# Performance work log

Hardware: AMD Instinct MI355X
Metric: run time of the kernel (lower is better)

Reference implementation:

```python
import jax, jax.numpy as jnp
import numpy as np

D_MODEL = 2048
N_HEADS = 16
HEAD_DIM = D_MODEL // N_HEADS  # 128


def setup_inputs() -> dict:
    key = jax.random.key(0)
    ks = jax.random.split(key, 7)
    B, S, CACHE = 2, 2048, 2048
    scale = 1.0 / np.sqrt(D_MODEL)
    return {
        "x": jax.random.normal(ks[0], (B, S, D_MODEL), dtype=jnp.float32),
        "cached_k": jax.random.normal(ks[1], (B, N_HEADS, CACHE, HEAD_DIM), dtype=jnp.float32),
        "cached_v": jax.random.normal(ks[2], (B, N_HEADS, CACHE, HEAD_DIM), dtype=jnp.float32),
        "W_q": jax.random.normal(ks[3], (D_MODEL, D_MODEL), dtype=jnp.float32) * scale,
        "W_k": jax.random.normal(ks[4], (D_MODEL, D_MODEL), dtype=jnp.float32) * scale,
        "W_v": jax.random.normal(ks[5], (D_MODEL, D_MODEL), dtype=jnp.float32) * scale,
        "W_o": jax.random.normal(ks[6], (D_MODEL, D_MODEL), dtype=jnp.float32) * scale,
    }


def reference(x, cached_k, cached_v, W_q, W_k, W_v, W_o):
    B, S, _ = x.shape
    # nn.Linear(d,d,bias=False): y = x @ W.T
    def proj(W):
        h = jnp.einsum("bsd,ed->bse", x, W)
        return h.reshape(B, S, N_HEADS, HEAD_DIM).transpose(0, 2, 1, 3)  # (B,H,S,Dh)
    q = proj(W_q)
    k = jnp.concatenate([cached_k, proj(W_k)], axis=2)  # (B,H,T,Dh)
    v = jnp.concatenate([cached_v, proj(W_v)], axis=2)
    scores = jnp.einsum("bhsd,bhtd->bhst", q, k) / np.sqrt(HEAD_DIM)
    attn = jax.nn.softmax(scores, axis=-1)
    out = jnp.einsum("bhst,bhtd->bhsd", attn, v)  # (B,H,S,Dh)
    out = out.transpose(0, 2, 1, 3).reshape(B, S, D_MODEL)
    out = jnp.einsum("bsd,ed->bse", out, W_o)
    return out, k, v
```

## Files before the change

### kernel.cpp

```cpp
#include <hip/hip_runtime.h>

typedef __bf16 bf16;
typedef __bf16 bf16x4 __attribute__((ext_vector_type(4)));
typedef __bf16 bf16x8 __attribute__((ext_vector_type(8)));
typedef float f32x4 __attribute__((ext_vector_type(4)));
typedef float f32x16 __attribute__((ext_vector_type(16)));
typedef int iv2 __attribute__((ext_vector_type(2)));

#define LOG2E 1.44269504088896340736f
#define QSCALE 0.12751884935f
#define RESCALE_THR 8.0f

__device__ __forceinline__ void gload_lds16(const void* gp, void* lp) {
    __builtin_amdgcn_global_load_lds(
        (__attribute__((address_space(1))) void*)gp,
        (__attribute__((address_space(3))) void*)lp,
        16, 0, 0);
}

__device__ __forceinline__ int kmask(int r) {
    return (r & 15) ^ (((r >> 5) & 1) << 2);
}

__device__ __forceinline__ unsigned cvtpk(float lo, float hi) {
    unsigned w;
    asm("v_cvt_pk_bf16_f32 %0, %1, %2" : "=v"(w) : "v"(lo), "v"(hi));
    return w;
}

__device__ __forceinline__ iv2 permswap(unsigned a, unsigned b) {
    return __builtin_amdgcn_permlane32_swap((int)a, (int)b, false, false);
}
__device__ __forceinline__ float halfmax(float v) {
    iv2 r = permswap(__float_as_uint(v), __float_as_uint(v));
    return fmaxf(__int_as_float(r[0]), __int_as_float(r[1]));
}
__device__ __forceinline__ float halfadd(float v) {
    iv2 r = permswap(__float_as_uint(v), __float_as_uint(v));
    return __int_as_float(r[0]) + __int_as_float(r[1]);
}

__device__ __forceinline__ float vmax32(const f32x16& a, const f32x16& b) {
    float t[8];
    #pragma unroll
    for (int i = 0; i < 8; ++i)
        t[i] = fmaxf(fmaxf(a[i], a[i + 8]), fmaxf(b[i], b[i + 8]));
    return fmaxf(fmaxf(fmaxf(t[0], t[1]), fmaxf(t[2], t[3])),
                 fmaxf(fmaxf(t[4], t[5]), fmaxf(t[6], t[7])));
}
__device__ __forceinline__ float vsum32(const f32x16& a, const f32x16& b) {
    float t[8];
    #pragma unroll
    for (int i = 0; i < 8; ++i)
        t[i] = (a[i] + a[i + 8]) + (b[i] + b[i + 8]);
    return ((t[0] + t[1]) + (t[2] + t[3])) + ((t[4] + t[5]) + (t[6] + t[7]));
}

__global__ void conv_all(const float* __restrict__ x, const float* __restrict__ wq,
                         const float* __restrict__ wk, const float* __restrict__ wv,
                         const float* __restrict__ wo, bf16* __restrict__ xb,
                         bf16* __restrict__ wbase) {
    int id = blockIdx.x;
    const float* src;
    bf16* dst;
    int i;
    if (id < 8192) {
        src = x; dst = xb;
        i = id * 256 + threadIdx.x;
    } else {
        int w = (id - 8192) >> 12;
        src = (w == 0) ? wq : (w == 1) ? wk : (w == 2) ? wv : wo;
        dst = wbase + (size_t)w * 4194304;
        i = ((id - 8192) & 4095) * 256 + threadIdx.x;
    }
    float4 f = ((const float4*)src)[i];
    bf16x4 v;
    v[0] = (bf16)f.x; v[1] = (bf16)f.y; v[2] = (bf16)f.z; v[3] = (bf16)f.w;
    *(bf16x4*)(dst + (size_t)i * 4) = v;
}

__global__ void copy_cache_k(const float* __restrict__ ck, float* __restrict__ kout,
                             bf16* __restrict__ kb) {
    size_t i = ((size_t)blockIdx.x * 256 + threadIdx.x) * 4;
    size_t bh  = i >> 18;
    size_t rem = i & 262143;
    size_t o   = (bh << 19) + rem;
    float4 f = *(const float4*)(ck + i);
    *(float4*)(kout + o) = f;
    bf16x4 v;
    v[0] = (bf16)f.x; v[1] = (bf16)f.y; v[2] = (bf16)f.z; v[3] = (bf16)f.w;
    *(bf16x4*)(kb + o) = v;
}

__global__ void copy_cache_v(const float* __restrict__ cv, float* __restrict__ vout,
                             bf16* __restrict__ vtb) {
    __shared__ float tile[32][33];
    int bh = blockIdx.z;
    int t0 = blockIdx.x * 32;
    int dh0 = blockIdx.y * 32;
    int tx = threadIdx.x, ty = threadIdx.y;
    const float* src = cv + (size_t)bh * 2048 * 128;
    float* dstf = vout + (size_t)bh * 4096 * 128;
    #pragma unroll
    for (int i = 0; i < 4; ++i) {
        int t = t0 + ty * 4 + i;
        float val = src[(size_t)t * 128 + dh0 + tx];
        dstf[(size_t)t * 128 + dh0 + tx] = val;
        tile[ty * 4 + i][tx] = val;
    }
    __syncthreads();
    bf16* dstb = vtb + (size_t)bh * 128 * 4096;
    #pragma unroll
    for (int i = 0; i < 4; ++i) {
        int dh = dh0 + ty * 4 + i;
        dstb[(size_t)dh * 4096 + t0 + tx] = (bf16)tile[tx][ty * 4 + i];
    }
}

__global__ void transpose_vnew(const float* __restrict__ vout, bf16* __restrict__ vtb) {
    __shared__ float tile[32][33];
    int bh = blockIdx.z;
    int t0 = 2048 + blockIdx.x * 32;
    int dh0 = blockIdx.y * 32;
    int tx = threadIdx.x, ty = threadIdx.y;
    const float* src = vout + (size_t)bh * 4096 * 128;
    #pragma unroll
    for (int i = 0; i < 4; ++i) {
        int t = t0 + ty * 4 + i;
        tile[ty * 4 + i][tx] = src[(size_t)t * 128 + dh0 + tx];
    }
    __syncthreads();
    bf16* dstb = vtb + (size_t)bh * 128 * 4096;
    #pragma unroll
    for (int i = 0; i < 4; ++i) {
        int dh = dh0 + ty * 4 + i;
        dstb[(size_t)dh * 4096 + t0 + tx] = (bf16)tile[tx][ty * 4 + i];
    }
}

__global__ __launch_bounds__(256)
void gemm_qkv(const bf16* __restrict__ A, const bf16* __restrict__ Bm,
              float* __restrict__ kout, float* __restrict__ vout,
              bf16* __restrict__ qb, bf16* __restrict__ kb) {
    const int K = 2048;
    __shared__ __align__(16) char smem[32768];
    const int tid = threadIdx.x;
    const int wid = tid >> 6;
    const int lane = tid & 63;
    const int quad = lane >> 4;
    const int l16 = lane & 15;
    const int wg = blockIdx.x;
    const int xcd = wg & 7;
    const int i_x = wg >> 3;
    const int m0 = (i_x / 6) * 128;
    const int n0 = (xcd * 6 + i_x % 6) * 128;
    const int wm = (wid & 1) * 64;
    const int wn = (wid >> 1) * 64;

    f32x4 zero = {0.f, 0.f, 0.f, 0.f};
    f32x4 acc[4][4];
    #pragma unroll
    for (int i = 0; i < 4; ++i)
        #pragma unroll
        for (int j = 0; j < 4; ++j) acc[i][j] = zero;

    auto stage = [&](int k0, int buf) {
        char* base = smem + buf * 16384;
        #pragma unroll
        for (int t = 0; t < 2; ++t) {
            int c = t * 256 + tid;
            int row = c >> 2, kc = c & 3;
            const char* gA = (const char*)(A + (size_t)(m0 + row) * K + k0 + kc * 8);
            const char* gB = (const char*)(Bm + (size_t)(n0 + row) * K + k0 + kc * 8);
            char* lA = smem + buf * 16384 + (size_t)(t * 256 + (tid & ~63)) * 16;
            char* lB = base + 8192 + (size_t)(t * 256 + (tid & ~63)) * 16;
            gload_lds16(gA, lA);
            gload_lds16(gB, lB);
        }
    };

    stage(0, 0);
    __syncthreads();

    for (int k0 = 0; k0 < K; k0 += 32) {
        const int cur = (k0 >> 5) & 1;
        if (k0 + 32 < K) stage(k0 + 32, cur ^ 1);
        const char* base = smem + cur * 16384;
        bf16x8 af[4], bfv[4];
        #pragma unroll
        for (int i = 0; i < 4; ++i) {
            af[i]  = *(const bf16x8*)(base + ((wm + i * 16 + l16) * 32 + quad * 8) * 2);
            bfv[i] = *(const bf16x8*)(base + 8192 + ((wn + i * 16 + l16) * 32 + quad * 8) * 2);
        }
        __builtin_amdgcn_s_setprio(1);
        #pragma unroll
        for (int i = 0; i < 4; ++i)
            #pragma unroll
            for (int j = 0; j < 4; ++j)
                acc[i][j] = __builtin_amdgcn_mfma_f32_16x16x32_bf16(af[i], bfv[j], acc[i][j], 0, 0, 0);
        __builtin_amdgcn_s_setprio(0);
        __syncthreads();
    }

    const int seg = n0 >> 11;
    #pragma unroll
    for (int i = 0; i < 4; ++i)
        #pragma unroll
        for (int j = 0; j < 4; ++j)
            #pragma unroll
            for (int r = 0; r < 4; ++r) {
                int grow = m0 + wm + i * 16 + quad * 4 + r;
                int gcol = n0 + wn + j * 16 + l16;
                float v = acc[i][j][r];
                int b = grow >> 11, s = grow & 2047;
                int c2 = gcol & 2047;
                int h = c2 >> 7, dh = c2 & 127;
                if (seg == 0) {
                    qb[(((size_t)(b * 16 + h) * 2048) + s) * 128 + dh] = (bf16)(v * QSCALE);
                } else if (seg == 1) {
                    size_t idx = (((size_t)(b * 16 + h) * 4096) + 2048 + s) * 128 + dh;
                    kout[idx] = v;
                    kb[idx] = (bf16)v;
                } else {
                    size_t idx = (((size_t)(b * 16 + h) * 4096) + 2048 + s) * 128 + dh;
                    vout[idx] = v;
                }
            }
}

__global__ __launch_bounds__(256)
void gemm_out(const bf16* __restrict__ A, const bf16* __restrict__ Bm,
              float* __restrict__ out_f32) {
    const int K = 2048, N = 2048;
    __shared__ __align__(16) char smem[32768];
    const int tid = threadIdx.x;
    const int wid = tid >> 6;
    const int lane = tid & 63;
    const int quad = lane >> 4;
    const int l16 = lane & 15;
    const int wg = blockIdx.x;
    const int xcd = wg & 7;
    const int i_x = wg >> 3;
    const int m0 = (i_x >> 1) * 128;
    const int n0 = (xcd * 2 + (i_x & 1)) * 128;
    const int wm = (wid & 1) * 64;
    const int wn = (wid >> 1) * 64;

    f32x4 zero = {0.f, 0.f, 0.f, 0.f};
    f32x4 acc[4][4];
    #pragma unroll
    for (int i = 0; i < 4; ++i)
        #pragma unroll
        for (int j = 0; j < 4; ++j) acc[i][j] = zero;

    auto stage = [&](int k0, int buf) {
        char* base = smem + buf * 16384;
        #pragma unroll
        for (int t = 0; t < 2; ++t) {
            int c = t * 256 + tid;
            int row = c >> 2, kc = c & 3;
            const char* gA = (const char*)(A + (size_t)(m0 + row) * K + k0 + kc * 8);
            const char* gB = (const char*)(Bm + (size_t)(n0 + row) * K + k0 + kc * 8);
            char* lA = base + (size_t)(t * 256 + (tid & ~63)) * 16;
            char* lB = base + 8192 + (size_t)(t * 256 + (tid & ~63)) * 16;
            gload_lds16(gA, lA);
            gload_lds16(gB, lB);
        }
    };

    stage(0, 0);
    __syncthreads();

    for (int k0 = 0; k0 < K; k0 += 32) {
        const int cur = (k0 >> 5) & 1;
        if (k0 + 32 < K) stage(k0 + 32, cur ^ 1);
        const char* base = smem + cur * 16384;
        bf16x8 af[4], bfv[4];
        #pragma unroll
        for (int i = 0; i < 4; ++i) {
            af[i]  = *(const bf16x8*)(base + ((wm + i * 16 + l16) * 32 + quad * 8) * 2);
            bfv[i] = *(const bf16x8*)(base + 8192 + ((wn + i * 16 + l16) * 32 + quad * 8) * 2);
        }
        __builtin_amdgcn_s_setprio(1);
        #pragma unroll
        for (int i = 0; i < 4; ++i)
            #pragma unroll
            for (int j = 0; j < 4; ++j)
                acc[i][j] = __builtin_amdgcn_mfma_f32_16x16x32_bf16(af[i], bfv[j], acc[i][j], 0, 0, 0);
        __builtin_amdgcn_s_setprio(0);
        __syncthreads();
    }

    #pragma unroll
    for (int i = 0; i < 4; ++i)
        #pragma unroll
        for (int j = 0; j < 4; ++j)
            #pragma unroll
            for (int r = 0; r < 4; ++r) {
                int grow = m0 + wm + i * 16 + quad * 4 + r;
                int gcol = n0 + wn + j * 16 + l16;
                out_f32[(size_t)grow * N + gcol] = acc[i][j][r];
            }
}

__global__ __launch_bounds__(256, 2)
void flash_attn(const bf16* __restrict__ qb, const bf16* __restrict__ kb,
                const bf16* __restrict__ vtb, bf16* __restrict__ ab) {
    __shared__ __align__(16) char smem[65536];
    const int tid = threadIdx.x;
    const int wid = tid >> 6;
    const int lane = tid & 63;
    const int hh = lane >> 5;
    const int l31 = lane & 31;

    const int flat = blockIdx.x;
    const int xcd = flat & 7;
    const int idx = flat >> 3;
    const int bh = xcd * 4 + (idx >> 4);
    const int qblk = idx & 15;
    const int b = bh >> 4, h = bh & 15;
    const int s0 = qblk * 128 + wid * 32;

    const bf16* Q  = qb  + (size_t)bh * 2048 * 128;
    const bf16* Kp = kb  + (size_t)bh * 4096 * 128;
    const bf16* Vt = vtb + (size_t)bh * 128 * 4096;

    bf16x8 qf[8];
    #pragma unroll
    for (int ks = 0; ks < 8; ++ks)
        qf[ks] = *(const bf16x8*)(Q + (size_t)(s0 + l31) * 128 + ks * 16 + hh * 8);

    f32x16 oacc[4];
    #pragma unroll
    for (int dhb = 0; dhb < 4; ++dhb)
        #pragma unroll
        for (int i = 0; i < 16; ++i) oacc[dhb][i] = 0.f;
    float mrun = -1e30f, lrun = 0.f;

    auto stage = [&](int t0, int buf) {
        char* Kb = smem + buf * 32768;
        char* Vb = Kb + 16384;
        #pragma unroll
        for (int r4 = 0; r4 < 4; ++r4) {
            int kc = r4 * 256 + tid;
            int row = kc >> 4, p = kc & 15;
            int j = p ^ kmask(row);
            gload_lds16(Kp + (size_t)(t0 + row) * 128 + j * 8, Kb + kc * 16);
        }
        #pragma unroll
        for (int r4 = 0; r4 < 4; ++r4) {
            int vc = r4 * 256 + tid;
            int row = vc >> 4, j = vc & 15;
            int g = j ^ kmask(row);
            int dh = row + (g >> 3) * 64;
            int p = g & 7;
            gload_lds16(Vt + (size_t)dh * 4096 + t0 + p * 8, Vb + vc * 16);
        }
    };

    stage(0, 0);
    __syncthreads();

    for (int t0 = 0; t0 < 4096; t0 += 64) {
        const int cur = (t0 >> 6) & 1;
        if (t0 + 64 < 4096) stage(t0 + 64, cur ^ 1);
        const char* Ksh = smem + cur * 32768;
        const char* Vsh = Ksh + 16384;

        f32x16 sacc[2];
        #pragma unroll
        for (int i = 0; i < 16; ++i) { sacc[0][i] = 0.f; sacc[1][i] = 0.f; }
        __builtin_amdgcn_s_setprio(1);
        #pragma unroll
        for (int ks = 0; ks < 8; ++ks) {
            const int c = ks * 2 + hh;
            const int r0 = l31, r1 = 32 + l31;
            bf16x8 kf0 = *(const bf16x8*)(Ksh + r0 * 256 + (c ^ kmask(r0)) * 16);
            bf16x8 kf1 = *(const bf16x8*)(Ksh + r1 * 256 + (c ^ kmask(r1)) * 16);
            sacc[0] = __builtin_amdgcn_mfma_f32_32x32x16_bf16(kf0, qf[ks], sacc[0], 0, 0, 0);
            sacc[1] = __builtin_amdgcn_mfma_f32_32x32x16_bf16(kf1, qf[ks], sacc[1], 0, 0, 0);
        }
        __builtin_amdgcn_s_setprio(0);

        float mx = halfmax(vmax32(sacc[0], sacc[1]));
        if (!__all(mx <= mrun + RESCALE_THR)) {
            float mnew = fmaxf(mrun, mx);
            float alpha = __builtin_amdgcn_exp2f(mrun - mnew);
            #pragma unroll
            for (int dhb = 0; dhb < 4; ++dhb)
                #pragma unroll
                for (int i = 0; i < 16; ++i) oacc[dhb][i] *= alpha;
            lrun *= alpha;
            mrun = mnew;
        }
        #pragma unroll
        for (int tb = 0; tb < 2; ++tb)
            #pragma unroll
            for (int i = 0; i < 16; ++i)
                sacc[tb][i] = __builtin_amdgcn_exp2f(sacc[tb][i] - mrun);
        lrun += halfadd(vsum32(sacc[0], sacc[1]));

        bf16x8 pf[4];
        #pragma unroll
        for (int tb = 0; tb < 2; ++tb)
            #pragma unroll
            for (int ksl = 0; ksl < 2; ++ksl) {
                const int g0 = ksl * 8;
                unsigned wa0 = cvtpk(sacc[tb][g0 + 0], sacc[tb][g0 + 1]);
                unsigned wb0 = cvtpk(sacc[tb][g0 + 4], sacc[tb][g0 + 5]);
                unsigned wa1 = cvtpk(sacc[tb][g0 + 2], sacc[tb][g0 + 3]);
                unsigned wb1 = cvtpk(sacc[tb][g0 + 6], sacc[tb][g0 + 7]);
                iv2 r0 = permswap(wa0, wb0);
                iv2 r1 = permswap(wa1, wb1);
                union { int u[4]; bf16x8 v; } pk;
                pk.u[0] = r0[0]; pk.u[1] = r1[0]; pk.u[2] = r0[1]; pk.u[3] = r1[1];
                pf[tb * 2 + ksl] = pk.v;
            }

        __builtin_amdgcn_s_setprio(1);
        #pragma unroll
        for (int dhb = 0; dhb < 4; ++dhb) {
            const int rr = ((dhb & 1) << 5) + l31;
            #pragma unroll
            for (int ks = 0; ks < 4; ++ks) {
                const int g = (dhb >> 1) * 8 + ks * 2 + hh;
                bf16x8 vf = *(const bf16x8*)(Vsh + rr * 256 + (g ^ kmask(rr)) * 16);
                oacc[dhb] = __builtin_amdgcn_mfma_f32_32x32x16_bf16(vf, pf[ks], oacc[dhb], 0, 0, 0);
            }
        }
        __builtin_amdgcn_s_setprio(0);

        __syncthreads();
    }

    const float inv = 1.0f / lrun;
    const int s = s0 + l31;
    #pragma unroll
    for (int dhb = 0; dhb < 4; ++dhb)
        #pragma unroll
        for (int g = 0; g < 4; ++g) {
            bf16x4 o4;
            #pragma unroll
            for (int r = 0; r < 4; ++r) o4[r] = (bf16)(oacc[dhb][g * 4 + r] * inv);
            int dh = dhb * 32 + g * 8 + hh * 4;
            *(bf16x4*)(ab + ((size_t)(b * 2048 + s)) * 2048 + h * 128 + dh) = o4;
        }
}

extern "C" void kernel_launch(void* const* d_in, const int* in_sizes, int n_in,
                              void* d_out, int out_size, void* d_ws, size_t ws_size,
                              hipStream_t stream) {
    const float* x        = (const float*)d_in[0];
    const float* cached_k = (const float*)d_in[1];
    const float* cached_v = (const float*)d_in[2];
    const float* W_q      = (const float*)d_in[3];
    const float* W_k      = (const float*)d_in[4];
    const float* W_v      = (const float*)d_in[5];
    const float* W_o      = (const float*)d_in[6];

    float* out  = (float*)d_out;
    float* kout = out + 8388608;
    float* vout = out + 25165824;

    char* ws = (char*)d_ws;
    size_t off = 0;
    auto alloc = [&](size_t elts) { bf16* p = (bf16*)(ws + off); off += elts * 2; return p; };
    bf16* xb  = alloc(8388608);
    bf16* wqb = alloc(4194304);
    bf16* wkb = alloc(4194304);
    bf16* wvb = alloc(4194304);
    bf16* wob = alloc(4194304);
    bf16* qb  = alloc(8388608);
    bf16* kb  = alloc(16777216);
    bf16* vtb = alloc(16777216);
    bf16* ab  = alloc(8388608);
    (void)wkb; (void)wvb;

    conv_all<<<24576, 256, 0, stream>>>(x, W_q, W_k, W_v, W_o, xb, wqb);
    copy_cache_k<<<8192, 256, 0, stream>>>(cached_k, kout, kb);
    copy_cache_v<<<dim3(64, 4, 32), dim3(32, 8), 0, stream>>>(cached_v, vout, vtb);

    gemm_qkv<<<1536, 256, 0, stream>>>(xb, wqb, kout, vout, qb, kb);
    transpose_vnew<<<dim3(64, 4, 32), dim3(32, 8), 0, stream>>>(vout, vtb);

    flash_attn<<<512, 256, 0, stream>>>(qb, kb, vtb, ab);

    gemm_out<<<512, 256, 0, stream>>>(ab, wob, out);
}
```

Baseline: 642.0 us.

## Enlarge QKV GEMM tiles to 256x256 with 4-stage swizzled LDS pipeline

Rewrites the fused QKV projection GEMM to use 256x256 block tiles with 8 waves (512 threads), each computing a 128x64 sub-tile. It replaces the double-buffered loop with a 4-slot ring buffer that prefetches two tiles ahead, using explicit vmcnt waits and a single barrier per iteration. It also XOR-swizzles the LDS layout to reduce bank conflicts. Larger tiles raise arithmetic intensity and reduce global traffic, but the grid shrinks to 384 blocks and register and LDS use grow, which may limit occupancy.

```diff
diff --git a/kernel.cpp b/kernel.cpp
--- a/kernel.cpp
+++ b/kernel.cpp
@@ -138,12 +138,12 @@
     }
 }
 
-__global__ __launch_bounds__(256)
+__global__ __launch_bounds__(512, 2)
 void gemm_qkv(const bf16* __restrict__ A, const bf16* __restrict__ Bm,
               float* __restrict__ kout, float* __restrict__ vout,
               bf16* __restrict__ qb, bf16* __restrict__ kb) {
-    const int K = 2048;
-    __shared__ __align__(16) char smem[32768];
+    const int K = 2048, NKT = 64;
+    __shared__ __align__(16) char smem[131072];
     const int tid = threadIdx.x;
     const int wid = tid >> 6;
     const int lane = tid & 63;
@@ -152,66 +152,87 @@
     const int wg = blockIdx.x;
     const int xcd = wg & 7;
     const int i_x = wg >> 3;
-    const int m0 = (i_x / 6) * 128;
-    const int n0 = (xcd * 6 + i_x % 6) * 128;
-    const int wm = (wid & 1) * 64;
-    const int wn = (wid >> 1) * 64;
+    const int m0 = (i_x / 3) * 256;
+    const int n0 = (xcd * 3 + i_x % 3) * 256;
+    const int wm = (wid >> 2) * 128;
+    const int wn = (wid & 3) * 64;
 
     f32x4 zero = {0.f, 0.f, 0.f, 0.f};
-    f32x4 acc[4][4];
-    #pragma unroll
-    for (int i = 0; i < 4; ++i)
+    f32x4 acc[8][4];
+    #pragma unroll
+    for (int i = 0; i < 8; ++i)
         #pragma unroll
         for (int j = 0; j < 4; ++j) acc[i][j] = zero;
 
-    auto stage = [&](int k0, int buf) {
-        char* base = smem + buf * 16384;
-        #pragma unroll
-        for (int t = 0; t < 2; ++t) {
-            int c = t * 256 + tid;
-            int row = c >> 2, kc = c & 3;
-            const char* gA = (const char*)(A + (size_t)(m0 + row) * K + k0 + kc * 8);
-            const char* gB = (const char*)(Bm + (size_t)(n0 + row) * K + k0 + kc * 8);
-            char* lA = smem + buf * 16384 + (size_t)(t * 256 + (tid & ~63)) * 16;
-            char* lB = base + 8192 + (size_t)(t * 256 + (tid & ~63)) * 16;
-            gload_lds16(gA, lA);
-            gload_lds16(gB, lB);
+    const int ldsw = (tid & ~63) * 16;
+
+    auto stage = [&](int kt) {
+        char* slot = smem + (kt & 3) * 32768;
+        const bf16* ga = A + (size_t)m0 * K + kt * 32;
+        const bf16* gb = Bm + (size_t)n0 * K + kt * 32;
+        #pragma unroll
+        for (int i = 0; i < 2; ++i) {
+            int c = i * 512 + tid;
+            int row = c >> 2, j = c & 3;
+            int jg = j ^ ((row >> 1) & 3);
+            gload_lds16(ga + (size_t)row * K + jg * 8, slot + ldsw + i * 8192);
+        }
+        #pragma unroll
+        for (int i = 0; i < 2; ++i) {
+            int c = i * 512 + tid;
+            int row = c >> 2, j = c & 3;
+            int jg = j ^ ((row >> 1) & 3);
+            gload_lds16(gb + (size_t)row * K + jg * 8, slot + 16384 + ldsw + i * 8192);
         }
     };
 
-    stage(0, 0);
-    __syncthreads();
-
-    for (int k0 = 0; k0 < K; k0 += 32) {
-        const int cur = (k0 >> 5) & 1;
-        if (k0 + 32 < K) stage(k0 + 32, cur ^ 1);
-        const char* base = smem + cur * 16384;
-        bf16x8 af[4], bfv[4];
-        #pragma unroll
-        for (int i = 0; i < 4; ++i) {
-            af[i]  = *(const bf16x8*)(base + ((wm + i * 16 + l16) * 32 + quad * 8) * 2);
-            bfv[i] = *(const bf16x8*)(base + 8192 + ((wn + i * 16 + l16) * 32 + quad * 8) * 2);
+    stage(0);
+    stage(1);
+
+    #pragma unroll 1
+    for (int kt = 0; kt < NKT; ++kt) {
+        if (kt + 2 < NKT) {
+            stage(kt + 2);
+            asm volatile("s_waitcnt vmcnt(8)" ::: "memory");
+        } else if (kt + 1 < NKT) {
+            asm volatile("s_waitcnt vmcnt(4)" ::: "memory");
+        } else {
+            asm volatile("s_waitcnt vmcnt(0)" ::: "memory");
+        }
+        __builtin_amdgcn_s_barrier();
+        asm volatile("" ::: "memory");
+
+        const char* slot = smem + (kt & 3) * 32768;
+        bf16x8 af[8], bfv[4];
+        #pragma unroll
+        for (int mi = 0; mi < 8; ++mi) {
+            int row = wm + mi * 16 + l16;
+            af[mi] = *(const bf16x8*)(slot + row * 64 + (quad ^ ((row >> 1) & 3)) * 16);
+        }
+        #pragma unroll
+        for (int ni = 0; ni < 4; ++ni) {
+            int row = wn + ni * 16 + l16;
+            bfv[ni] = *(const bf16x8*)(slot + 16384 + row * 64 + (quad ^ ((row >> 1) & 3)) * 16);
         }
         __builtin_amdgcn_s_setprio(1);
         #pragma unroll
-        for (int i = 0; i < 4; ++i)
-            #pragma unroll
-            for (int j = 0; j < 4; ++j)
-                acc[i][j] = __builtin_amdgcn_mfma_f32_16x16x32_bf16(af[i], bfv[j], acc[i][j], 0, 0, 0);
+        for (int mi = 0; mi < 8; ++mi)
+            #pragma unroll
+            for (int ni = 0; ni < 4; ++ni)
+                acc[mi][ni] = __builtin_amdgcn_mfma_f32_16x16x32_bf16(af[mi], bfv[ni], acc[mi][ni], 0, 0, 0);
         __builtin_amdgcn_s_setprio(0);
-        __syncthreads();
     }
 
     const int seg = n0 >> 11;
     #pragma unroll
-    for (int i = 0; i < 4; ++i)
-        #pragma unroll
-        for (int j = 0; j < 4; ++j)
+    for (int mi = 0; mi < 8; ++mi)
+        #pragma unroll
+        for (int ni = 0; ni < 4; ++ni)
             #pragma unroll
             for (int r = 0; r < 4; ++r) {
-                int grow = m0 + wm + i * 16 + quad * 4 + r;
-                int gcol = n0 + wn + j * 16 + l16;
-                float v = acc[i][j][r];
+                int grow = m0 + wm + mi * 16 + quad * 4 + r;
+                int gcol = n0 + wn + ni * 16 + l16;
+                float v = acc[mi][ni][r];
                 int b = grow >> 11, s = grow & 2047;
                 int c2 = gcol & 2047;
                 int h = c2 >> 7, dh = c2 & 127;
@@ -480,7 +501,7 @@
     copy_cache_k<<<8192, 256, 0, stream>>>(cached_k, kout, kb);
     copy_cache_v<<<dim3(64, 4, 32), dim3(32, 8), 0, stream>>>(cached_v, vout, vtb);
 
-    gemm_qkv<<<1536, 256, 0, stream>>>(xb, wqb, kout, vout, qb, kb);
+    gemm_qkv<<<384, 512, 0, stream>>>(xb, wqb, kout, vout, qb, kb);
     transpose_vnew<<<dim3(64, 4, 32), dim3(32, 8), 0, stream>>>(vout, vtb);
 
     flash_attn<<<512, 256, 0, stream>>>(qb, kb, vtb, ab);
```

Measured after the change: 628.4 us. 2.1% less time.
